# Performance work log

Hardware: AMD Instinct MI355X
Metric: run time of the kernel (lower is better)

The kernel has to match this reference:

```python
import jax, jax.numpy as jnp
import numpy as np

WAY = 5
EPS = 1e-12  # torch F.normalize eps


def setup_inputs() -> dict:
    key = jax.random.key(0)
    k1, k2, k3, k4 = jax.random.split(key, 4)
    n_support, n_queries = 25, 200
    f_g, f_l, d = 16, 64, 512
    return {
        "support_set_global": jax.random.normal(k1, (n_support, f_g, d), jnp.float32),
        "support_set_local": jax.random.normal(k2, (n_support, f_l, d), jnp.float32),
        "support_labels": (jnp.arange(n_support) % WAY).astype(jnp.int64),
        "queries_global": jax.random.normal(k3, (n_queries, f_g, d), jnp.float32),
        "queries_local": jax.random.normal(k4, (n_queries, f_l, d), jnp.float32),
    }


def _l2norm(x):
    # torch F.normalize(dim=1) with eps clamp
    n = jnp.linalg.norm(x, axis=-1, keepdims=True)
    return x / jnp.maximum(n, EPS)


def reference(support_set_global, support_set_local, support_labels,
              queries_global, queries_local):
    # Dropout is identity in eval mode; omitted for a deterministic reference.
    S = jnp.concatenate([support_set_global, support_set_local], axis=1)  # [nS, F, D]
    Q = jnp.concatenate([queries_global, queries_local], axis=1)          # [nQ, F, D]
    nS, F, D = S.shape
    nQ = Q.shape[0]

    Sn = _l2norm(S.reshape(nS * F, D))
    Qn = _l2norm(Q.reshape(nQ * F, D))

    # cosine-sim matmul: [nS*F, nQ*F]
    sim = Sn @ Qn.T
    # view(nS, F, nQ, F).transpose(2,1) -> [nS, nQ, F, F]
    sim = sim.reshape(nS, F, nQ, F).transpose(0, 2, 1, 3)
    dmat = 1.0 - sim

    # squared Frobenius norm over last two dims, keepdim -> [nS, nQ, 1, 1]
    fro2 = jnp.sum(dmat * dmat, axis=(-2, -1))  # [nS, nQ]
    # dists.min(3)[0].sum(2) + dists.min(2)[0].sum(2) over singleton dims == 2 * fro2
    cum_dists = 2.0 * fro2  # [nS, nQ]

    # per-class mean over support rows (class-wise gather-mean)
    counts = jax.ops.segment_sum(jnp.ones((nS,), cum_dists.dtype), support_labels,
                                 num_segments=WAY)                       # [WAY]
    class_sum = jax.ops.segment_sum(cum_dists, support_labels, num_segments=WAY)  # [WAY, nQ]
    class_dists = class_sum / counts[:, None]

    logits = -class_dists.T  # [nQ, WAY]
    return logits
```

## Files before the change

kernel.cpp:

```cpp
#include <hip/hip_runtime.h>

#define NS 25
#define NQ 200
#define FG 16
#define FL 64
#define FTOT 80
#define D 512
#define WAY 5
#define MROWS 2000
#define MPAD 2080
#define NROWS 16000

typedef unsigned char u8;
typedef __attribute__((ext_vector_type(4))) float floatx4;
typedef __attribute__((ext_vector_type(4))) int intx4;

__device__ inline void gload_lds16(const void* g, void* l) {
    __builtin_amdgcn_global_load_lds(
        (const __attribute__((address_space(1))) unsigned int*)g,
        (__attribute__((address_space(3))) unsigned int*)l, 16, 0, 0);
}

__global__ __launch_bounds__(256) void normalize_kernel(
        const float* __restrict__ sg, const float* __restrict__ sl,
        const float* __restrict__ qg, const float* __restrict__ ql,
        u8* __restrict__ Sn, u8* __restrict__ Qn,
        const int* __restrict__ labels,
        float* __restrict__ out, float* __restrict__ rcnt) {
    if (blockIdx.x == 1125) {
        intx4 z = {0, 0, 0, 0};
        intx4* pad = (intx4*)(Sn + (size_t)MROWS * D);
        for (int i = threadIdx.x; i < (MPAD - MROWS) * D / 16; i += 256) pad[i] = z;
        for (int i = threadIdx.x; i < NQ * WAY; i += 256) out[i] = 0.f;
        if (threadIdx.x == 0) {
            int counts[WAY] = {0, 0, 0, 0, 0};
            for (int s = 0; s < NS; ++s) counts[labels[s]]++;
            for (int c = 0; c < WAY; ++c) rcnt[c] = 1.0f / (float)(counts[c] ? counts[c] : 1);
        }
        return;
    }
    const int wv = (blockIdx.x * blockDim.x + threadIdx.x) >> 6;
    const int lane = threadIdx.x & 63;
    const int row0 = wv * 4;

    const float* srcs[4];
    u8* dsts[4];
    #pragma unroll
    for (int k = 0; k < 4; ++k) {
        const int row = row0 + k;
        if (row < MROWS) {
            const int s = row / FTOT, f = row % FTOT;
            srcs[k] = (f < FG) ? sg + (size_t)(s * FG + f) * D
                               : sl + (size_t)(s * FL + (f - FG)) * D;
            dsts[k] = Sn + (size_t)row * D;
        } else {
            const int r = row - MROWS;
            const int q = r / FTOT, f = r % FTOT;
            srcs[k] = (f < FG) ? qg + (size_t)(q * FG + f) * D
                               : ql + (size_t)(q * FL + (f - FG)) * D;
            dsts[k] = Qn + (size_t)r * D;
        }
    }

    float4 va[4], vb[4];
    #pragma unroll
    for (int k = 0; k < 4; ++k) {
        va[k] = ((const float4*)srcs[k])[2 * lane];
        vb[k] = ((const float4*)srcs[k])[2 * lane + 1];
    }

    float ss[4];
    #pragma unroll
    for (int k = 0; k < 4; ++k)
        ss[k] = va[k].x*va[k].x + va[k].y*va[k].y + va[k].z*va[k].z + va[k].w*va[k].w
              + vb[k].x*vb[k].x + vb[k].y*vb[k].y + vb[k].z*vb[k].z + vb[k].w*vb[k].w;

    #pragma unroll
    for (int off = 32; off > 0; off >>= 1) {
        #pragma unroll
        for (int k = 0; k < 4; ++k) ss[k] += __shfl_xor(ss[k], off, 64);
    }

    #pragma unroll
    for (int k = 0; k < 4; ++k) {
        const float scale = 1.0f / fmaxf(sqrtf(ss[k]), 1e-12f);
        int w0 = __builtin_amdgcn_cvt_pk_fp8_f32(va[k].x * scale, va[k].y * scale, 0, false);
        w0     = __builtin_amdgcn_cvt_pk_fp8_f32(va[k].z * scale, va[k].w * scale, w0, true);
        int w1 = __builtin_amdgcn_cvt_pk_fp8_f32(vb[k].x * scale, vb[k].y * scale, 0, false);
        w1     = __builtin_amdgcn_cvt_pk_fp8_f32(vb[k].z * scale, vb[k].w * scale, w1, true);
        ((int2*)dsts[k])[lane] = make_int2(w0, w1);
    }
}

__global__ __launch_bounds__(256, 3) void gemm_kernel(const u8* __restrict__ Sn,
                                                      const u8* __restrict__ Qn,
                                                      const int* __restrict__ labels,
                                                      const float* __restrict__ rcnt,
                                                      float* __restrict__ out) {
    __shared__ u8 As[160][128];
    __shared__ u8 Bs[160][128];

    const int bx = blockIdx.x;
    const int by = blockIdx.y;
    const int tid = threadIdx.x;
    const int lane = tid & 63;
    const int w = tid >> 6;
    const int lm = lane & 15;
    const int lq = lane >> 4;
    const int wr = w >> 1;
    const int wc = w & 1;

    floatx4 acc[5][5];
    #pragma unroll
    for (int i = 0; i < 5; ++i)
        #pragma unroll
        for (int j = 0; j < 5; ++j) acc[i][j] = (floatx4){0.f, 0.f, 0.f, 0.f};

    const u8* Sbase = Sn + (size_t)by * 160 * D;
    const u8* Qbase = Qn + (size_t)bx * 160 * D;

    const u8* gsrc = (w < 2) ? Sbase : Qbase;
    u8* ldst = (w < 2) ? (u8*)As : (u8*)Bs;
    const int sl0 = (w & 1) * 10;
    const int grow = lane >> 3;
    const int gc = lane & 7;

    #pragma unroll 1
    for (int kc = 0; kc < 4; ++kc) {
        const int k0 = kc * 128;
        __syncthreads();
        #pragma unroll
        for (int t = 0; t < 10; ++t) {
            const int sl = sl0 + t;
            const int r = sl * 8 + grow;
            const int cp = gc ^ ((r >> 1) & 7);
            gload_lds16(gsrc + (size_t)r * D + k0 + cp * 16, ldst + sl * 1024);
        }
        __syncthreads();
        #pragma unroll
        for (int ks = 0; ks < 4; ++ks) {
            long long a[5], b[5];
            #pragma unroll
            for (int i = 0; i < 5; ++i) {
                const int r = wr * 80 + i * 16 + lm;
                const int c = (ks * 2 + (lq >> 1)) ^ ((r >> 1) & 7);
                a[i] = *(const long long*)(&As[r][c * 16 + (lq & 1) * 8]);
            }
            #pragma unroll
            for (int j = 0; j < 5; ++j) {
                const int r = wc * 80 + j * 16 + lm;
                const int c = (ks * 2 + (lq >> 1)) ^ ((r >> 1) & 7);
                b[j] = *(const long long*)(&Bs[r][c * 16 + (lq & 1) * 8]);
            }
            #pragma unroll
            for (int i = 0; i < 5; ++i)
                #pragma unroll
                for (int j = 0; j < 5; ++j)
                    acc[i][j] = __builtin_amdgcn_mfma_f32_16x16x32_fp8_fp8(a[i], b[j], acc[i][j], 0, 0, 0);
        }
    }

    float local = 0.f;
    #pragma unroll
    for (int i = 0; i < 5; ++i)
        #pragma unroll
        for (int j = 0; j < 5; ++j)
            #pragma unroll
            for (int r = 0; r < 4; ++r) {
                const float d = 1.0f - acc[i][j][r];
                local = fmaf(d, d, local);
            }
    #pragma unroll
    for (int off = 32; off > 0; off >>= 1) local += __shfl_down(local, off, 64);

    const int sIdx = by * 2 + wr;
    const int qIdx = bx * 2 + wc;
    if (lane == 0 && sIdx < NS) {
        const int c = labels[sIdx];
        atomicAdd(&out[qIdx * WAY + c], -2.0f * local * rcnt[c]);
    }
}

extern "C" void kernel_launch(void* const* d_in, const int* in_sizes, int n_in,
                              void* d_out, int out_size, void* d_ws, size_t ws_size,
                              hipStream_t stream) {
    const float* sg = (const float*)d_in[0];
    const float* sl = (const float*)d_in[1];
    const int* labels = (const int*)d_in[2];
    const float* qg = (const float*)d_in[3];
    const float* ql = (const float*)d_in[4];
    float* out = (float*)d_out;

    u8* Sn = (u8*)d_ws;
    u8* Qn = Sn + (size_t)MPAD * D;
    float* rcnt = (float*)(Qn + (size_t)NROWS * D);

    normalize_kernel<<<1126, 256, 0, stream>>>(sg, sl, qg, ql, Sn, Qn, labels, out, rcnt);
    dim3 g2(100, 13);
    gemm_kernel<<<g2, 256, 0, stream>>>(Sn, Qn, labels, rcnt, out);
}
```

Baseline: 111.1 us.

## Switch GEMM to 128x128 tiles with scaled 16x16x128 FP8 MFMA and XCD-aware grid

The GEMM tile shrinks from 160x160 to 128x128, and the 16x16x32 FP8 MFMA is replaced with the MI355X scaled 16x16x128 f8f6f4 MFMA at unit scale. Each 128-wide K chunk now needs a single MFMA per output fragment. Because the tiles no longer line up with the 80-row sample boundaries, the epilogue splits each wave's partial sums into up to four sample-pair buckets and issues several atomics. The grid becomes a 1D launch swizzled across the 8 XCDs, with tiles past the end exiting early. The intent is fewer MFMA issues and better L2 locality, at the cost of more atomics, padding waste and tile-to-sample bookkeeping.

Measured after the change: 115.8 us. 1.04x slower.

```diff
diff --git a/kernel.cpp b/kernel.cpp
--- a/kernel.cpp
+++ b/kernel.cpp
@@ -8,12 +8,13 @@
 #define D 512
 #define WAY 5
 #define MROWS 2000
-#define MPAD 2080
+#define MPAD 2048
 #define NROWS 16000
 
 typedef unsigned char u8;
 typedef __attribute__((ext_vector_type(4))) float floatx4;
 typedef __attribute__((ext_vector_type(4))) int intx4;
+typedef __attribute__((ext_vector_type(8))) int intx8;
 
 __device__ inline void gload_lds16(const void* g, void* l) {
     __builtin_amdgcn_global_load_lds(
@@ -97,11 +98,15 @@
                                                       const int* __restrict__ labels,
                                                       const float* __restrict__ rcnt,
                                                       float* __restrict__ out) {
-    __shared__ u8 As[160][128];
-    __shared__ u8 Bs[160][128];
-
-    const int bx = blockIdx.x;
-    const int by = blockIdx.y;
+    __shared__ __align__(16) u8 As[128][128];
+    __shared__ __align__(16) u8 Bs[128][128];
+
+    const int t = blockIdx.x;
+    const int pos = t >> 3;
+    const int bx = (t & 7) * 16 + (pos & 15);
+    const int by = pos >> 4;
+    if (bx >= 125) return;
+
     const int tid = threadIdx.x;
     const int lane = tid & 63;
     const int w = tid >> 6;
@@ -110,74 +115,113 @@
     const int wr = w >> 1;
     const int wc = w & 1;
 
-    floatx4 acc[5][5];
-    #pragma unroll
-    for (int i = 0; i < 5; ++i)
-        #pragma unroll
-        for (int j = 0; j < 5; ++j) acc[i][j] = (floatx4){0.f, 0.f, 0.f, 0.f};
-
-    const u8* Sbase = Sn + (size_t)by * 160 * D;
-    const u8* Qbase = Qn + (size_t)bx * 160 * D;
+    floatx4 acc[4][4];
+    #pragma unroll
+    for (int i = 0; i < 4; ++i)
+        #pragma unroll
+        for (int j = 0; j < 4; ++j) acc[i][j] = (floatx4){0.f, 0.f, 0.f, 0.f};
+
+    const u8* Sbase = Sn + (size_t)by * 128 * D;
+    const u8* Qbase = Qn + (size_t)bx * 128 * D;
 
     const u8* gsrc = (w < 2) ? Sbase : Qbase;
     u8* ldst = (w < 2) ? (u8*)As : (u8*)Bs;
-    const int sl0 = (w & 1) * 10;
+    const int sl0 = (w & 1) * 8;
     const int grow = lane >> 3;
     const int gc = lane & 7;
+
+    union frag { intx8 v; intx4 h[2]; };
+
+    int aoff[4], boff[4];
+    #pragma unroll
+    for (int i = 0; i < 4; ++i) {
+        const int ra = wr * 64 + i * 16 + lm;
+        aoff[i] = ra * 128 + (((2 * lq) ^ ((ra >> 1) & 7)) * 16);
+        const int rb = wc * 64 + i * 16 + lm;
+        boff[i] = rb * 128 + (((2 * lq) ^ ((rb >> 1) & 7)) * 16);
+    }
 
     #pragma unroll 1
     for (int kc = 0; kc < 4; ++kc) {
         const int k0 = kc * 128;
         __syncthreads();
         #pragma unroll
-        for (int t = 0; t < 10; ++t) {
-            const int sl = sl0 + t;
+        for (int u = 0; u < 8; ++u) {
+            const int sl = sl0 + u;
             const int r = sl * 8 + grow;
             const int cp = gc ^ ((r >> 1) & 7);
             gload_lds16(gsrc + (size_t)r * D + k0 + cp * 16, ldst + sl * 1024);
         }
         __syncthreads();
-        #pragma unroll
-        for (int ks = 0; ks < 4; ++ks) {
-            long long a[5], b[5];
+
+        frag af[4];
+        #pragma unroll
+        for (int i = 0; i < 4; ++i) {
+            af[i].h[0] = *(const intx4*)((const u8*)As + aoff[i]);
+            af[i].h[1] = *(const intx4*)((const u8*)As + (aoff[i] ^ 16));
+        }
+        #pragma unroll
+        for (int j = 0; j < 4; ++j) {
+            frag bf;
+            bf.h[0] = *(const intx4*)((const u8*)Bs + boff[j]);
+            bf.h[1] = *(const intx4*)((const u8*)Bs + (boff[j] ^ 16));
             #pragma unroll
-            for (int i = 0; i < 5; ++i) {
-                const int r = wr * 80 + i * 16 + lm;
-                const int c = (ks * 2 + (lq >> 1)) ^ ((r >> 1) & 7);
-                a[i] = *(const long long*)(&As[r][c * 16 + (lq & 1) * 8]);
-            }
-            #pragma unroll
-            for (int j = 0; j < 5; ++j) {
-                const int r = wc * 80 + j * 16 + lm;
-                const int c = (ks * 2 + (lq >> 1)) ^ ((r >> 1) & 7);
-                b[j] = *(const long long*)(&Bs[r][c * 16 + (lq & 1) * 8]);
-            }
-            #pragma unroll
-            for (int i = 0; i < 5; ++i)
-                #pragma unroll
-                for (int j = 0; j < 5; ++j)
-                    acc[i][j] = __builtin_amdgcn_mfma_f32_16x16x32_fp8_fp8(a[i], b[j], acc[i][j], 0, 0, 0);
-        }
-    }
-
-    float local = 0.f;
-    #pragma unroll
-    for (int i = 0; i < 5; ++i)
-        #pragma unroll
-        for (int j = 0; j < 5; ++j)
+            for (int i = 0; i < 4; ++i)
+                acc[i][j] = __builtin_amdgcn_mfma_scale_f32_16x16x128_f8f6f4(
+                    af[i].v, bf.v, acc[i][j], 0, 0,
+                    0, 0x7F7F7F7F, 0, 0x7F7F7F7F);
+        }
+    }
+
+    const int R0 = by * 128 + wr * 64;
+    const int C0 = bx * 128 + wc * 64;
+    const int s0 = R0 / 80;
+    const int q0 = C0 / 80;
+    int rsplit = (s0 + 1) * 80 - R0; if (rsplit > 64) rsplit = 64;
+    int csplit = (q0 + 1) * 80 - C0; if (csplit > 64) csplit = 64;
+
+    float l00 = 0.f, l01 = 0.f, l10 = 0.f, l11 = 0.f;
+    const int rowb = (lane >> 4) * 4;
+    const int colb = lane & 15;
+    #pragma unroll
+    for (int i = 0; i < 4; ++i)
+        #pragma unroll
+        for (int j = 0; j < 4; ++j) {
+            const int lcol = j * 16 + colb;
             #pragma unroll
             for (int r = 0; r < 4; ++r) {
+                const int lrow = i * 16 + rowb + r;
                 const float d = 1.0f - acc[i][j][r];
-                local = fmaf(d, d, local);
+                const float dd = d * d;
+                if (lrow < rsplit) { if (lcol < csplit) l00 += dd; else l01 += dd; }
+                else               { if (lcol < csplit) l10 += dd; else l11 += dd; }
             }
-    #pragma unroll
-    for (int off = 32; off > 0; off >>= 1) local += __shfl_down(local, off, 64);
-
-    const int sIdx = by * 2 + wr;
-    const int qIdx = bx * 2 + wc;
-    if (lane == 0 && sIdx < NS) {
-        const int c = labels[sIdx];
-        atomicAdd(&out[qIdx * WAY + c], -2.0f * local * rcnt[c]);
+        }
+
+    #pragma unroll
+    for (int off = 32; off > 0; off >>= 1) {
+        l00 += __shfl_down(l00, off, 64);
+        l01 += __shfl_down(l01, off, 64);
+        l10 += __shfl_down(l10, off, 64);
+        l11 += __shfl_down(l11, off, 64);
+    }
+
+    if (lane == 0) {
+        #pragma unroll
+        for (int si = 0; si < 2; ++si) {
+            const int s = s0 + si;
+            if (si == 1 && rsplit >= 64) continue;
+            if (s >= NS) continue;
+            const int c = labels[s];
+            const float rc = -2.0f * rcnt[c];
+            #pragma unroll
+            for (int qi = 0; qi < 2; ++qi) {
+                if (qi == 1 && csplit >= 64) continue;
+                const int q = q0 + qi;
+                const float v = si ? (qi ? l11 : l10) : (qi ? l01 : l00);
+                atomicAdd(&out[q * WAY + c], v * rc);
+            }
+        }
     }
 }
 
@@ -196,6 +240,5 @@
     float* rcnt = (float*)(Qn + (size_t)NROWS * D);
 
     normalize_kernel<<<1126, 256, 0, stream>>>(sg, sl, qg, ql, Sn, Qn, labels, out, rcnt);
-    dim3 g2(100, 13);
-    gemm_kernel<<<g2, 256, 0, stream>>>(Sn, Qn, labels, rcnt, out);
-}
+    gemm_kernel<<<2048, 256, 0, stream>>>(Sn, Qn, labels, rcnt, out);
+}
```
